# Kernel tuning notes

Hardware: AMD Instinct MI355X
Metric: run time of the kernel (lower is better)

The kernel has to match this reference:

```python
import jax, jax.numpy as jnp
import numpy as np

K = 3; PAD = 1; CIN = 64; COUT = 64; B = 4; H = 128; W = 128


def setup_inputs() -> dict:
    key = jax.random.key(0)
    k1, k2, k3 = jax.random.split(key, 3)
    x = jax.random.normal(k1, (B, CIN, H, W), dtype=jnp.float32)
    # offset-predicting conv: [2*K*K, Cin, K, K]; small init -> sub-pixel offsets
    w_off = jax.random.normal(k2, (2 * K * K, CIN, K, K), dtype=jnp.float32) * 0.01
    b_off = jnp.zeros((2 * K * K,), dtype=jnp.float32)
    # deformable conv weight (bias=False): [Cout, Cin, K, K]
    w_def = jax.random.normal(k3, (COUT, CIN, K, K), dtype=jnp.float32) * 0.05
    return {"x": x, "w_off": w_off, "b_off": b_off, "w_def": w_def}


def _deform_conv(x, w_off, b_off, w_def):
    Bb, Cin, Hh, Ww = x.shape
    KK = K * K
    # 1) predict offsets with a regular 3x3 conv (stride 1, pad 1)
    off = jax.lax.conv_general_dilated(
        x, w_off, window_strides=(1, 1), padding=[(PAD, PAD), (PAD, PAD)],
        dimension_numbers=("NCHW", "OIHW", "NCHW"))
    off = off + b_off[None, :, None, None]          # [B, 2*KK, H, W]
    off = off.reshape(Bb, KK, 2, Hh, Ww)            # torchvision layout: (dy, dx) per tap
    dy, dx = off[:, :, 0], off[:, :, 1]             # [B, KK, H, W]

    # 2) sampling coordinates: p = p0 + p_k + offset
    ky = (jnp.arange(KK) // K).astype(x.dtype)
    kx = (jnp.arange(KK) % K).astype(x.dtype)
    hh = jnp.arange(Hh, dtype=x.dtype)
    ww = jnp.arange(Ww, dtype=x.dtype)
    py = hh[None, None, :, None] - PAD + ky[None, :, None, None] + dy   # [B,KK,H,W]
    px = ww[None, None, None, :] - PAD + kx[None, :, None, None] + dx

    # 3) bilinear sampling with zero padding outside the image
    y0f = jnp.floor(py); x0f = jnp.floor(px)
    fy = py - y0f; fx = px - x0f
    y0 = y0f.astype(jnp.int32); x0 = x0f.astype(jnp.int32)
    x_flat = x.reshape(Bb, Cin, Hh * Ww)

    def gather(yi, xi):
        valid = (yi >= 0) & (yi < Hh) & (xi >= 0) & (xi < Ww)
        idx = jnp.clip(yi, 0, Hh - 1) * Ww + jnp.clip(xi, 0, Ww - 1)     # [B,KK,H,W]
        g = jax.vmap(lambda xf, ix: xf[:, ix.reshape(-1)])(x_flat, idx)  # [B,Cin,KK*H*W]
        return g.reshape(Bb, Cin, KK, Hh, Ww) * valid[:, None].astype(x.dtype)

    sampled = (gather(y0, x0)         * ((1 - fy) * (1 - fx))[:, None]
             + gather(y0, x0 + 1)     * ((1 - fy) * fx)[:, None]
             + gather(y0 + 1, x0)     * (fy * (1 - fx))[:, None]
             + gather(y0 + 1, x0 + 1) * (fy * fx)[:, None])               # [B,Cin,KK,H,W]

    # 4) convolution accumulation over (Cin, kernel taps)
    return jnp.einsum('bckhw,ock->bohw', sampled, w_def.reshape(COUT, Cin, KK))


def reference(x, w_off, b_off, w_def):
    return _deform_conv(x, w_off, b_off, w_def)
```

## Files before the change

kernel.cpp:

```cpp
#include <hip/hip_runtime.h>
#include <hip/hip_fp16.h>

#define Bn   4
#define CINc 64
#define COUTc 64
#define Hn   128
#define Wn   128
#define HW   (Hn * Wn)
#define KKc  9
#define NOFF 18

typedef short bf16x8 __attribute__((ext_vector_type(8)));
typedef float f32x4  __attribute__((ext_vector_type(4)));
typedef float f32x2  __attribute__((ext_vector_type(2)));

__device__ inline unsigned short f2bf(float f) {
    unsigned int u = __float_as_uint(f);
    return (unsigned short)((u + 0x7fffu + ((u >> 16) & 1u)) >> 16);
}

__device__ inline void dma16(const void* g, void* l) {
#if __has_builtin(__builtin_amdgcn_global_load_lds)
    __builtin_amdgcn_global_load_lds(
        (__attribute__((address_space(1))) void*)(g),
        (__attribute__((address_space(3))) void*)(l), 16, 0, 0);
#else
    *(uint4*)l = *(const uint4*)g;
#endif
}

__global__ __launch_bounds__(256) void prep_all(
        const float* __restrict__ x, unsigned short* __restrict__ xt,
        const float* __restrict__ w_off, const float* __restrict__ w_def,
        unsigned short* __restrict__ wkb_sw, unsigned short* __restrict__ wob_sw) {
    int gb = blockIdx.x;
    int t  = threadIdx.x;
    if (gb < 1024) {
        __shared__ float s[64][65];
        int half = gb & 1;
        int h    = (gb >> 1) & 127;
        int b    = gb >> 8;
        int w0   = half * 64;

        const float* xb = x + (size_t)b * CINc * HW + (size_t)h * Wn + w0;
        int c0 = t >> 4, wq = (t & 15) * 4;
        #pragma unroll
        for (int i = 0; i < 4; ++i) {
            int c = c0 + i * 16;
            float4 v = *(const float4*)(xb + (size_t)c * HW + wq);
            s[c][wq]     = v.x;
            s[c][wq + 1] = v.y;
            s[c][wq + 2] = v.z;
            s[c][wq + 3] = v.w;
        }
        __syncthreads();

        int cpair = t & 31, pxg = t >> 5;
        unsigned* xtp = (unsigned*)xt;
        #pragma unroll
        for (int i = 0; i < 8; ++i) {
            int px = pxg * 8 + i;
            float v0 = s[cpair * 2][px], v1 = s[cpair * 2 + 1][px];
            unsigned d = (unsigned)f2bf(v0) | ((unsigned)f2bf(v1) << 16);
            xtp[(((size_t)(b * Hn + h) * Wn) + w0 + px) * 32 + cpair] = d;
        }
        return;
    }
    int idx = (gb - 1024) * 256 + t;
    if (idx < 36864) {
        int j = idx & 7, l = (idx >> 3) & 63, s = idx >> 9;
        int k = s >> 3, kc = (s >> 2) & 1, ot = s & 3;
        int l15 = l & 15, quad = l >> 4;
        int o = ot * 16 + l15, c = kc * 32 + quad * 8 + j;
        wkb_sw[idx] = f2bf(w_def[((size_t)o * 64 + c) * 9 + k]);
    }
    int i2 = idx - 36864;
    if (i2 >= 0 && i2 < 18432) {
        int j = i2 & 7, l = (i2 >> 3) & 63, s = i2 >> 9;
        int tt = s >> 2, kc = (s >> 1) & 1, mt = s & 1;
        int l15 = l & 15, quad = l >> 4;
        int m = mt * 16 + l15, c = kc * 32 + quad * 8 + j;
        unsigned short v = 0;
        if (m < NOFF) v = f2bf(w_off[((size_t)m * 64 + c) * 9 + tt]);
        wob_sw[i2] = v;
    }
}


#define BFBUILD(C, kc, BF, W0, W1, W2, W3)                                   \
    do {                                                                     \
        const unsigned* t0 = (const unsigned*)&(C)[(kc) * 4 + 0];            \
        const unsigned* t1 = (const unsigned*)&(C)[(kc) * 4 + 1];            \
        const unsigned* b0 = (const unsigned*)&(C)[(kc) * 4 + 2];            \
        const unsigned* b1 = (const unsigned*)&(C)[(kc) * 4 + 3];            \
        _Pragma("unroll")                                                    \
        for (int jd = 0; jd < 4; ++jd) {                                     \
            f32x2 t0p = {__uint_as_float(t0[jd] << 16),                      \
                         __uint_as_float(t0[jd] & 0xFFFF0000u)};             \
            f32x2 t1p = {__uint_as_float(t1[jd] << 16),                      \
                         __uint_as_float(t1[jd] & 0xFFFF0000u)};             \
            f32x2 b0p = {__uint_as_float(b0[jd] << 16),                      \
                         __uint_as_float(b0[jd] & 0xFFFF0000u)};             \
            f32x2 b1p = {__uint_as_float(b1[jd] << 16),                      \
                         __uint_as_float(b1[jd] & 0xFFFF0000u)};             \
            f32x2 vv = t0p * (W0) + t1p * (W1) + b0p * (W2) + b1p * (W3);    \
            unsigned pk;                                                     \
            asm("v_cvt_pk_bf16_f32 %0, %1, %2"                               \
                : "=v"(pk) : "v"(vv.x), "v"(vv.y));                          \
            (BF).u[jd] = pk;                                                 \
        }                                                                    \
    } while (0)

#define TAP(k)                                                               \
    do {                                                                     \
        const uint4* C = R[(k) & 1];                                         \
        union { unsigned u; __half2 hv; } c01, c23;                          \
        c01.u = pw01[(k)]; c23.u = pw23[(k)];                                \
        float W0 = __low2float(c01.hv), W1 = __high2float(c01.hv);           \
        float W2 = __low2float(c23.hv), W3 = __high2float(c23.hv);           \
        union { bf16x8 v; unsigned u[4]; } bfa, bfb;                         \
        BFBUILD(C, 0, bfa, W0, W1, W2, W3);                                  \
        BFBUILD(C, 1, bfb, W0, W1, W2, W3);                                  \
        _Pragma("unroll")                                                    \
        for (int ot = 0; ot < 4; ++ot) {                                     \
            bf16x8 af0 = s_w[(((k) * 2 + 0) * 4 + ot + 36) * 64 + lane];     \
            acc[ot] = __builtin_amdgcn_mfma_f32_16x16x32_bf16(               \
                af0, bfa.v, acc[ot], 0, 0, 0);                               \
            bf16x8 af1 = s_w[(((k) * 2 + 1) * 4 + ot + 36) * 64 + lane];     \
            acc[ot] = __builtin_amdgcn_mfma_f32_16x16x32_bf16(               \
                af1, bfb.v, acc[ot], 0, 0, 0);                               \
        }                                                                    \
    } while (0)

#define FETCH(kk, st)                                                \
    do {                                                             \
        unsigned ad_ = ad[kk];                                       \
        unsigned xc_ = ad_ >> 16;                                    \
        unsigned at_ = (((ad_ & 255u) << 7) + xc_) << 6;             \
        unsigned ab_ = ((((ad_ >> 8) & 255u) << 7) + xc_) << 6;      \
        R[st][0] = *(const uint4*)(xtb + at_ + co0);                 \
        R[st][1] = *(const uint4*)(xtb + at_ + 64 + co0);            \
        R[st][2] = *(const uint4*)(xtb + ab_ + co0);                 \
        R[st][3] = *(const uint4*)(xtb + ab_ + 64 + co0);            \
        R[st][4] = *(const uint4*)(xtb + at_ + co1);                 \
        R[st][5] = *(const uint4*)(xtb + at_ + 64 + co1);            \
        R[st][6] = *(const uint4*)(xtb + ab_ + co1);                 \
        R[st][7] = *(const uint4*)(xtb + ab_ + 64 + co1);            \
    } while (0)

__global__ __launch_bounds__(512, 2) void fused_deform_v19(
        const unsigned short* __restrict__ xt,
        const unsigned short* __restrict__ wob_sw,
        const unsigned short* __restrict__ wkb_sw,
        const float* __restrict__ b_off, float* __restrict__ out) {
    extern __shared__ bf16x8 s_w[];

    int gid  = blockIdx.x;
    int tid  = threadIdx.x;
    int lane = tid & 63;
    int wave = __builtin_amdgcn_readfirstlane(tid >> 6);
    int l15  = lane & 15;
    int quad = lane >> 4;

    #pragma unroll
    for (int i = 0; i < 14; ++i) {
        int seg = i * 8 + wave;
        if (seg < 108) {
            const uint4* src = (seg < 36)
                ? (const uint4*)wob_sw + (size_t)seg * 64 + lane
                : (const uint4*)wkb_sw + (size_t)(seg - 36) * 64 + lane;
            dma16(src, (char*)s_w + (size_t)seg * 1024);
        }
    }

    bool first = true;
    #pragma unroll 1
    for (int row = 0; row < 2; ++row) {
        int gv   = gid + row * 256;
        int xcd  = gv & 7;
        int j    = gv >> 3;
        int hh   = j & 15;
        int b    = j >> 4;
        int h    = xcd * 16 + hh;
        int p    = wave * 16 + l15;

        uint4 L[9][2];
        unsigned msk[9];
        const unsigned short* xtb = xt + (size_t)b * HW * 64;
        #pragma unroll
        for (int t9 = 0; t9 < 9; ++t9) {
            int ty = t9 / 3, tx = t9 % 3;
            int y  = h - 1 + ty;
            int xg = p - 1 + tx;
            bool v = (y >= 0) && (y < Hn) && (xg >= 0) && (xg < Wn);
            msk[t9] = v ? 0xFFFFFFFFu : 0u;
            int yc = min(max(y, 0), Hn - 1);
            int xc = min(max(xg, 0), Wn - 1);
            size_t base = ((size_t)yc * Wn + xc) * 64;
            L[t9][0] = *(const uint4*)(xtb + base + quad * 8);
            L[t9][1] = *(const uint4*)(xtb + base + 32 + quad * 8);
        }
        if (first) {
            __syncthreads();
            first = false;
        }

        f32x4 oa0 = (f32x4){0.f, 0.f, 0.f, 0.f};
        f32x4 oa1 = (f32x4){0.f, 0.f, 0.f, 0.f};
        #pragma unroll
        for (int t9 = 0; t9 < 9; ++t9) {
            unsigned m = msk[t9];
            #pragma unroll
            for (int kc = 0; kc < 2; ++kc) {
                union { bf16x8 v; uint4 u; } bf;
                bf.u = L[t9][kc];
                bf.u.x &= m; bf.u.y &= m; bf.u.z &= m; bf.u.w &= m;
                bf16x8 a0 = s_w[((t9 * 2 + kc) * 2 + 0) * 64 + lane];
                bf16x8 a1 = s_w[((t9 * 2 + kc) * 2 + 1) * 64 + lane];
                oa0 = __builtin_amdgcn_mfma_f32_16x16x32_bf16(a0, bf.v, oa0, 0, 0, 0);
                oa1 = __builtin_amdgcn_mfma_f32_16x16x32_bf16(a1, bf.v, oa1, 0, 0, 0);
            }
        }

        unsigned my_ad[3]  = {0, 0, 0};
        unsigned my_w01[3] = {0, 0, 0};
        unsigned my_w23[3] = {0, 0, 0};
        auto phase1 = [&](int k, float dy, float dx, int slot) {
            float py  = (float)(h - 1 + k / 3) + dy;
            float pxf = (float)(p - 1 + k % 3) + dx;
            float y0f = floorf(py), x0f = floorf(pxf);
            float fy = py - y0f, fx = pxf - x0f;
            int y0 = (int)y0f, x0 = (int)x0f;
            bool vy0 = (y0 >= 0) & (y0 < Hn);
            bool vy1 = (y0 + 1 >= 0) & (y0 + 1 < Hn);
            bool vx0 = (x0 >= 0) & (x0 < Wn);
            bool vx1 = (x0 + 1 >= 0) & (x0 + 1 < Wn);
            float wy0 = vy0 ? 1.f - fy : 0.f;
            float wy1 = vy1 ? fy : 0.f;
            float wx0 = vx0 ? 1.f - fx : 0.f;
            float wx1 = vx1 ? fx : 0.f;
            int xc = min(max(x0, 0), Wn - 2);
            bool sel0 = (min(max(x0, 0), Wn - 1) != xc);
            bool sel1 = ((min(max(x0 + 1, 0), Wn - 1) - xc) == 1);
            float Wa = (sel0 ? 0.f : wx0) + (sel1 ? 0.f : wx1);
            float Wb = (sel0 ? wx0 : 0.f) + (sel1 ? wx1 : 0.f);
            int yc0 = min(max(y0, 0), Hn - 1), yc1 = min(max(y0 + 1, 0), Hn - 1);
            union { __half2 hv; unsigned u; } c01, c23;
            c01.hv = __floats2half2_rn(wy0 * Wa, wy0 * Wb);
            c23.hv = __floats2half2_rn(wy1 * Wa, wy1 * Wb);
            my_ad[slot]  = (unsigned)yc0 | ((unsigned)yc1 << 8) | ((unsigned)xc << 16);
            my_w01[slot] = c01.u;
            my_w23[slot] = c23.u;
        };
        int kb = quad * 2;
        phase1(kb,     oa0[0] + b_off[4 * quad],     oa0[1] + b_off[4 * quad + 1], 0);
        phase1(kb + 1, oa0[2] + b_off[4 * quad + 2], oa0[3] + b_off[4 * quad + 3], 1);
        if (quad == 0)
            phase1(8, oa1[0] + b_off[16], oa1[1] + b_off[17], 2);

        unsigned ad[KKc], pw01[KKc], pw23[KKc];
        #pragma unroll
        for (int k = 0; k < KKc; ++k) {
            int src  = (k < 8) ? ((k >> 1) * 16 + l15) : l15;
            int slot = (k < 8) ? (k & 1) : 2;
            ad[k]   = (unsigned)__shfl((int)my_ad[slot],  src, 64);
            pw01[k] = (unsigned)__shfl((int)my_w01[slot], src, 64);
            pw23[k] = (unsigned)__shfl((int)my_w23[slot], src, 64);
        }

        f32x4 acc[4];
        #pragma unroll
        for (int ot = 0; ot < 4; ++ot) acc[ot] = (f32x4){0.f, 0.f, 0.f, 0.f};

        uint4 R[2][8];
        int co0 = quad * 8, co1 = 32 + quad * 8;

        FETCH(0, 0);
        FETCH(1, 1); TAP(0);
        FETCH(2, 0); TAP(1);
        FETCH(3, 1); TAP(2);
        FETCH(4, 0); TAP(3);
        FETCH(5, 1); TAP(4);
        FETCH(6, 0); TAP(5);
        FETCH(7, 1); TAP(6);
        FETCH(8, 0); TAP(7);
        TAP(8);

        #pragma unroll
        for (int ot = 0; ot < 4; ++ot)
            #pragma unroll
            for (int rr = 0; rr < 4; ++rr) {
                int o = ot * 16 + quad * 4 + rr;
                out[(((size_t)b * COUTc + o) * Hn + h) * Wn + p] = acc[ot][rr];
            }
    }
}

extern "C" void kernel_launch(void* const* d_in, const int* in_sizes, int n_in,
                              void* d_out, int out_size, void* d_ws, size_t ws_size,
                              hipStream_t stream) {
    const float* x     = (const float*)d_in[0];
    const float* w_off = (const float*)d_in[1];
    const float* b_off = (const float*)d_in[2];
    const float* w_def = (const float*)d_in[3];
    float* out = (float*)d_out;

    char* ws = (char*)d_ws;
    unsigned short* xt = (unsigned short*)ws;
    ws += (size_t)Bn * HW * CINc * sizeof(unsigned short);
    unsigned short* wkb_sw = (unsigned short*)ws;
    ws += 36864 * sizeof(unsigned short);
    unsigned short* wob_sw = (unsigned short*)ws;

    static bool attr_set = false;
    if (!attr_set) {
        (void)hipFuncSetAttribute((const void*)fused_deform_v19,
                                  hipFuncAttributeMaxDynamicSharedMemorySize,
                                  110592);
        attr_set = true;
    }

    prep_all<<<1024 + 216, 256, 0, stream>>>(x, xt, w_off, w_def, wkb_sw, wob_sw);
    fused_deform_v19<<<256, 512, 110592, stream>>>(xt, wob_sw, wkb_sw, b_off, out);
}
```

Baseline: 116.5 us.

## Stage 5-row input halo in LDS and gather bilinear samples from shared memory

Each block now processes one output row and first copies a swizzled 5-row x 128-column x 64-channel bf16 halo of the input into LDS via async DMA. Both the offset conv and the deformable sampling read from LDS. A wave-level check falls back to global gathers when any sampled row lies outside the halo. The offset-conv weights and deform weights now share one LDS region that is reloaded between phases. LDS use grows to 152 KB, which likely means one block per CU, and the block count doubles with no row loop inside each block.

```diff
diff --git a/kernel.cpp b/kernel.cpp
--- a/kernel.cpp
+++ b/kernel.cpp
@@ -123,16 +123,16 @@
         BFBUILD(C, 1, bfb, W0, W1, W2, W3);                                  \
         _Pragma("unroll")                                                    \
         for (int ot = 0; ot < 4; ++ot) {                                     \
-            bf16x8 af0 = s_w[(((k) * 2 + 0) * 4 + ot + 36) * 64 + lane];     \
+            bf16x8 af0 = s_wv[(((k) * 2 + 0) * 4 + ot) * 64 + lane];         \
             acc[ot] = __builtin_amdgcn_mfma_f32_16x16x32_bf16(               \
                 af0, bfa.v, acc[ot], 0, 0, 0);                               \
-            bf16x8 af1 = s_w[(((k) * 2 + 1) * 4 + ot + 36) * 64 + lane];     \
+            bf16x8 af1 = s_wv[(((k) * 2 + 1) * 4 + ot) * 64 + lane];         \
             acc[ot] = __builtin_amdgcn_mfma_f32_16x16x32_bf16(               \
                 af1, bfb.v, acc[ot], 0, 0, 0);                               \
         }                                                                    \
     } while (0)
 
-#define FETCH(kk, st)                                                \
+#define FETCH_G(kk, st)                                              \
     do {                                                             \
         unsigned ad_ = ad[kk];                                       \
         unsigned xc_ = ad_ >> 16;                                    \
@@ -148,152 +148,202 @@
         R[st][7] = *(const uint4*)(xtb + ab_ + 64 + co1);            \
     } while (0)
 
-__global__ __launch_bounds__(512, 2) void fused_deform_v19(
+#define FETCH_L(kk, st)                                              \
+    do {                                                             \
+        unsigned ad_ = ad[kk];                                       \
+        int xc_ = (int)(ad_ >> 16);                                  \
+        int r0_ = (int)(ad_ & 255u) - h + 2;                         \
+        int r1_ = (int)((ad_ >> 8) & 255u) - h + 2;                  \
+        int b00 = (r0_ * 128 + xc_) * 128;                           \
+        int b10 = (r1_ * 128 + xc_) * 128;                           \
+        int j0  = (quad ^ (xc_ & 7)) << 4;                           \
+        int j1  = (quad ^ ((xc_ + 1) & 7)) << 4;                     \
+        int j0b = ((4 + quad) ^ (xc_ & 7)) << 4;                     \
+        int j1b = ((4 + quad) ^ ((xc_ + 1) & 7)) << 4;               \
+        R[st][0] = *(const uint4*)(s_mem + b00 + j0);                \
+        R[st][1] = *(const uint4*)(s_mem + b00 + 128 + j1);          \
+        R[st][2] = *(const uint4*)(s_mem + b10 + j0);                \
+        R[st][3] = *(const uint4*)(s_mem + b10 + 128 + j1);          \
+        R[st][4] = *(const uint4*)(s_mem + b00 + j0b);               \
+        R[st][5] = *(const uint4*)(s_mem + b00 + 128 + j1b);         \
+        R[st][6] = *(const uint4*)(s_mem + b10 + j0b);               \
+        R[st][7] = *(const uint4*)(s_mem + b10 + 128 + j1b);         \
+    } while (0)
+
+__global__ __launch_bounds__(512, 2) void fused_deform_v20(
         const unsigned short* __restrict__ xt,
         const unsigned short* __restrict__ wob_sw,
         const unsigned short* __restrict__ wkb_sw,
         const float* __restrict__ b_off, float* __restrict__ out) {
-    extern __shared__ bf16x8 s_w[];
+    extern __shared__ char s_mem[];
+    bf16x8* s_wv = (bf16x8*)(s_mem + 81920);
 
     int gid  = blockIdx.x;
+    int xcd  = gid & 7;
+    int j    = gid >> 3;
+    int hh   = j & 15;
+    int b    = j >> 4;
+    int h    = xcd * 16 + hh;
     int tid  = threadIdx.x;
     int lane = tid & 63;
     int wave = __builtin_amdgcn_readfirstlane(tid >> 6);
     int l15  = lane & 15;
     int quad = lane >> 4;
-
-    #pragma unroll
-    for (int i = 0; i < 14; ++i) {
+    int p    = wave * 16 + l15;
+
+    const unsigned short* xtb = xt + (size_t)b * HW * 64;
+
+    int xl = lane >> 3;
+    int sl = lane & 7;
+    #pragma unroll
+    for (int i = 0; i < 10; ++i) {
+        int slot = i * 8 + wave;
+        int r  = slot >> 4;
+        int g  = slot & 15;
+        int y  = min(max(h - 2 + r, 0), Hn - 1);
+        int xx = g * 8 + xl;
+        int jj = sl ^ (xx & 7);
+        dma16(xtb + ((size_t)y * Wn + xx) * 64 + jj * 8,
+              s_mem + (size_t)r * 16384 + (size_t)g * 1024);
+    }
+    #pragma unroll
+    for (int i = 0; i < 5; ++i) {
         int seg = i * 8 + wave;
-        if (seg < 108) {
-            const uint4* src = (seg < 36)
-                ? (const uint4*)wob_sw + (size_t)seg * 64 + lane
-                : (const uint4*)wkb_sw + (size_t)(seg - 36) * 64 + lane;
-            dma16(src, (char*)s_w + (size_t)seg * 1024);
+        if (seg < 36)
+            dma16((const uint4*)wob_sw + seg * 64 + lane,
+                  s_mem + 81920 + (size_t)seg * 1024);
+    }
+    __syncthreads();
+
+    f32x4 oa0 = (f32x4){0.f, 0.f, 0.f, 0.f};
+    f32x4 oa1 = (f32x4){0.f, 0.f, 0.f, 0.f};
+    #pragma unroll
+    for (int t9 = 0; t9 < 9; ++t9) {
+        int ty = t9 / 3, tx = t9 % 3;
+        int y  = h - 1 + ty;
+        int xg = p - 1 + tx;
+        bool v = (y >= 0) && (y < Hn) && (xg >= 0) && (xg < Wn);
+        unsigned m = v ? 0xFFFFFFFFu : 0u;
+        int yc = min(max(y, 0), Hn - 1);
+        int xc = min(max(xg, 0), Wn - 1);
+        int r  = yc - h + 2;
+        int base = (r * 128 + xc) * 128;
+        uint4 L0 = *(const uint4*)(s_mem + base + ((quad ^ (xc & 7)) << 4));
+        uint4 L1 = *(const uint4*)(s_mem + base + (((4 + quad) ^ (xc & 7)) << 4));
+        #pragma unroll
+        for (int kc = 0; kc < 2; ++kc) {
+            union { bf16x8 v; uint4 u; } bf;
+            bf.u = kc ? L1 : L0;
+            bf.u.x &= m; bf.u.y &= m; bf.u.z &= m; bf.u.w &= m;
+            bf16x8 a0 = s_wv[((t9 * 2 + kc) * 2 + 0) * 64 + lane];
+            bf16x8 a1 = s_wv[((t9 * 2 + kc) * 2 + 1) * 64 + lane];
+            oa0 = __builtin_amdgcn_mfma_f32_16x16x32_bf16(a0, bf.v, oa0, 0, 0, 0);
+            oa1 = __builtin_amdgcn_mfma_f32_16x16x32_bf16(a1, bf.v, oa1, 0, 0, 0);
         }
     }
 
-    bool first = true;
-    #pragma unroll 1
-    for (int row = 0; row < 2; ++row) {
-        int gv   = gid + row * 256;
-        int xcd  = gv & 7;
-        int j    = gv >> 3;
-        int hh   = j & 15;
-        int b    = j >> 4;
-        int h    = xcd * 16 + hh;
-        int p    = wave * 16 + l15;
-
-        uint4 L[9][2];
-        unsigned msk[9];
-        const unsigned short* xtb = xt + (size_t)b * HW * 64;
+    unsigned my_ad[3]  = {0, 0, 0};
+    unsigned my_w01[3] = {0, 0, 0};
+    unsigned my_w23[3] = {0, 0, 0};
+    auto phase1 = [&](int k, float dy, float dx, int slot) {
+        float py  = (float)(h - 1 + k / 3) + dy;
+        float pxf = (float)(p - 1 + k % 3) + dx;
+        float y0f = floorf(py), x0f = floorf(pxf);
+        float fy = py - y0f, fx = pxf - x0f;
+        int y0 = (int)y0f, x0 = (int)x0f;
+        bool vy0 = (y0 >= 0) & (y0 < Hn);
+        bool vy1 = (y0 + 1 >= 0) & (y0 + 1 < Hn);
+        bool vx0 = (x0 >= 0) & (x0 < Wn);
+        bool vx1 = (x0 + 1 >= 0) & (x0 + 1 < Wn);
+        float wy0 = vy0 ? 1.f - fy : 0.f;
+        float wy1 = vy1 ? fy : 0.f;
+        float wx0 = vx0 ? 1.f - fx : 0.f;
+        float wx1 = vx1 ? fx : 0.f;
+        int xc = min(max(x0, 0), Wn - 2);
+        bool sel0 = (min(max(x0, 0), Wn - 1) != xc);
+        bool sel1 = ((min(max(x0 + 1, 0), Wn - 1) - xc) == 1);
+        float Wa = (sel0 ? 0.f : wx0) + (sel1 ? 0.f : wx1);
+        float Wb = (sel0 ? wx0 : 0.f) + (sel1 ? wx1 : 0.f);
+        int yc0 = min(max(y0, 0), Hn - 1), yc1 = min(max(y0 + 1, 0), Hn - 1);
+        union { __half2 hv; unsigned u; } c01, c23;
+        c01.hv = __floats2half2_rn(wy0 * Wa, wy0 * Wb);
+        c23.hv = __floats2half2_rn(wy1 * Wa, wy1 * Wb);
+        my_ad[slot]  = (unsigned)yc0 | ((unsigned)yc1 << 8) | ((unsigned)xc << 16);
+        my_w01[slot] = c01.u;
+        my_w23[slot] = c23.u;
+    };
+    int kb = quad * 2;
+    phase1(kb,     oa0[0] + b_off[4 * quad],     oa0[1] + b_off[4 * quad + 1], 0);
+    phase1(kb + 1, oa0[2] + b_off[4 * quad + 2], oa0[3] + b_off[4 * quad + 3], 1);
+    if (quad == 0)
+        phase1(8, oa1[0] + b_off[16], oa1[1] + b_off[17], 2);
+    __syncthreads();
+
+    #pragma unroll
+    for (int i = 0; i < 9; ++i) {
+        int seg = i * 8 + wave;
+        dma16((const uint4*)wkb_sw + (size_t)seg * 64 + lane,
+              s_mem + 81920 + (size_t)seg * 1024);
+    }
+
+    unsigned ad[KKc], pw01[KKc], pw23[KKc];
+    #pragma unroll
+    for (int k = 0; k < KKc; ++k) {
+        int src  = (k < 8) ? ((k >> 1) * 16 + l15) : l15;
+        int slot = (k < 8) ? (k & 1) : 2;
+        ad[k]   = (unsigned)__shfl((int)my_ad[slot],  src, 64);
+        pw01[k] = (unsigned)__shfl((int)my_w01[slot], src, 64);
+        pw23[k] = (unsigned)__shfl((int)my_w23[slot], src, 64);
+    }
+    __syncthreads();
+
+    bool oow = false;
+    #pragma unroll
+    for (int k = 0; k < KKc; ++k) {
+        int r0 = (int)(ad[k] & 255u) - h + 2;
+        int r1 = (int)((ad[k] >> 8) & 255u) - h + 2;
+        oow |= ((unsigned)r0 > 4u) | ((unsigned)r1 > 4u);
+    }
+    bool use_global = __any(oow);
+
+    f32x4 acc[4];
+    #pragma unroll
+    for (int ot = 0; ot < 4; ++ot) acc[ot] = (f32x4){0.f, 0.f, 0.f, 0.f};
+
+    uint4 R[2][8];
+    int co0 = quad * 8, co1 = 32 + quad * 8;
+
+    if (__builtin_expect(use_global, 0)) {
+        FETCH_G(0, 0);
+        FETCH_G(1, 1); TAP(0);
+        FETCH_G(2, 0); TAP(1);
+        FETCH_G(3, 1); TAP(2);
+        FETCH_G(4, 0); TAP(3);
+        FETCH_G(5, 1); TAP(4);
+        FETCH_G(6, 0); TAP(5);
+        FETCH_G(7, 1); TAP(6);
+        FETCH_G(8, 0); TAP(7);
+        TAP(8);
+    } else {
+        FETCH_L(0, 0);
+        FETCH_L(1, 1); TAP(0);
+        FETCH_L(2, 0); TAP(1);
+        FETCH_L(3, 1); TAP(2);
+        FETCH_L(4, 0); TAP(3);
+        FETCH_L(5, 1); TAP(4);
+        FETCH_L(6, 0); TAP(5);
+        FETCH_L(7, 1); TAP(6);
+        FETCH_L(8, 0); TAP(7);
+        TAP(8);
+    }
+
+    #pragma unroll
+    for (int ot = 0; ot < 4; ++ot)
         #pragma unroll
-        for (int t9 = 0; t9 < 9; ++t9) {
-            int ty = t9 / 3, tx = t9 % 3;
-            int y  = h - 1 + ty;
-            int xg = p - 1 + tx;
-            bool v = (y >= 0) && (y < Hn) && (xg >= 0) && (xg < Wn);
-            msk[t9] = v ? 0xFFFFFFFFu : 0u;
-            int yc = min(max(y, 0), Hn - 1);
-            int xc = min(max(xg, 0), Wn - 1);
-            size_t base = ((size_t)yc * Wn + xc) * 64;
-            L[t9][0] = *(const uint4*)(xtb + base + quad * 8);
-            L[t9][1] = *(const uint4*)(xtb + base + 32 + quad * 8);
+        for (int rr = 0; rr < 4; ++rr) {
+            int o = ot * 16 + quad * 4 + rr;
+            out[(((size_t)b * COUTc + o) * Hn + h) * Wn + p] = acc[ot][rr];
         }
-        if (first) {
-            __syncthreads();
-            first = false;
-        }
-
-        f32x4 oa0 = (f32x4){0.f, 0.f, 0.f, 0.f};
-        f32x4 oa1 = (f32x4){0.f, 0.f, 0.f, 0.f};
-        #pragma unroll
-        for (int t9 = 0; t9 < 9; ++t9) {
-            unsigned m = msk[t9];
-            #pragma unroll
-            for (int kc = 0; kc < 2; ++kc) {
-                union { bf16x8 v; uint4 u; } bf;
-                bf.u = L[t9][kc];
-                bf.u.x &= m; bf.u.y &= m; bf.u.z &= m; bf.u.w &= m;
-                bf16x8 a0 = s_w[((t9 * 2 + kc) * 2 + 0) * 64 + lane];
-                bf16x8 a1 = s_w[((t9 * 2 + kc) * 2 + 1) * 64 + lane];
-                oa0 = __builtin_amdgcn_mfma_f32_16x16x32_bf16(a0, bf.v, oa0, 0, 0, 0);
-                oa1 = __builtin_amdgcn_mfma_f32_16x16x32_bf16(a1, bf.v, oa1, 0, 0, 0);
-            }
-        }
-
-        unsigned my_ad[3]  = {0, 0, 0};
-        unsigned my_w01[3] = {0, 0, 0};
-        unsigned my_w23[3] = {0, 0, 0};
-        auto phase1 = [&](int k, float dy, float dx, int slot) {
-            float py  = (float)(h - 1 + k / 3) + dy;
-            float pxf = (float)(p - 1 + k % 3) + dx;
-            float y0f = floorf(py), x0f = floorf(pxf);
-            float fy = py - y0f, fx = pxf - x0f;
-            int y0 = (int)y0f, x0 = (int)x0f;
-            bool vy0 = (y0 >= 0) & (y0 < Hn);
-            bool vy1 = (y0 + 1 >= 0) & (y0 + 1 < Hn);
-            bool vx0 = (x0 >= 0) & (x0 < Wn);
-            bool vx1 = (x0 + 1 >= 0) & (x0 + 1 < Wn);
-            float wy0 = vy0 ? 1.f - fy : 0.f;
-            float wy1 = vy1 ? fy : 0.f;
-            float wx0 = vx0 ? 1.f - fx : 0.f;
-            float wx1 = vx1 ? fx : 0.f;
-            int xc = min(max(x0, 0), Wn - 2);
-            bool sel0 = (min(max(x0, 0), Wn - 1) != xc);
-            bool sel1 = ((min(max(x0 + 1, 0), Wn - 1) - xc) == 1);
-            float Wa = (sel0 ? 0.f : wx0) + (sel1 ? 0.f : wx1);
-            float Wb = (sel0 ? wx0 : 0.f) + (sel1 ? wx1 : 0.f);
-            int yc0 = min(max(y0, 0), Hn - 1), yc1 = min(max(y0 + 1, 0), Hn - 1);
-            union { __half2 hv; unsigned u; } c01, c23;
-            c01.hv = __floats2half2_rn(wy0 * Wa, wy0 * Wb);
-            c23.hv = __floats2half2_rn(wy1 * Wa, wy1 * Wb);
-            my_ad[slot]  = (unsigned)yc0 | ((unsigned)yc1 << 8) | ((unsigned)xc << 16);
-            my_w01[slot] = c01.u;
-            my_w23[slot] = c23.u;
-        };
-        int kb = quad * 2;
-        phase1(kb,     oa0[0] + b_off[4 * quad],     oa0[1] + b_off[4 * quad + 1], 0);
-        phase1(kb + 1, oa0[2] + b_off[4 * quad + 2], oa0[3] + b_off[4 * quad + 3], 1);
-        if (quad == 0)
-            phase1(8, oa1[0] + b_off[16], oa1[1] + b_off[17], 2);
-
-        unsigned ad[KKc], pw01[KKc], pw23[KKc];
-        #pragma unroll
-        for (int k = 0; k < KKc; ++k) {
-            int src  = (k < 8) ? ((k >> 1) * 16 + l15) : l15;
-            int slot = (k < 8) ? (k & 1) : 2;
-            ad[k]   = (unsigned)__shfl((int)my_ad[slot],  src, 64);
-            pw01[k] = (unsigned)__shfl((int)my_w01[slot], src, 64);
-            pw23[k] = (unsigned)__shfl((int)my_w23[slot], src, 64);
-        }
-
-        f32x4 acc[4];
-        #pragma unroll
-        for (int ot = 0; ot < 4; ++ot) acc[ot] = (f32x4){0.f, 0.f, 0.f, 0.f};
-
-        uint4 R[2][8];
-        int co0 = quad * 8, co1 = 32 + quad * 8;
-
-        FETCH(0, 0);
-        FETCH(1, 1); TAP(0);
-        FETCH(2, 0); TAP(1);
-        FETCH(3, 1); TAP(2);
-        FETCH(4, 0); TAP(3);
-        FETCH(5, 1); TAP(4);
-        FETCH(6, 0); TAP(5);
-        FETCH(7, 1); TAP(6);
-        FETCH(8, 0); TAP(7);
-        TAP(8);
-
-        #pragma unroll
-        for (int ot = 0; ot < 4; ++ot)
-            #pragma unroll
-            for (int rr = 0; rr < 4; ++rr) {
-                int o = ot * 16 + quad * 4 + rr;
-                out[(((size_t)b * COUTc + o) * Hn + h) * Wn + p] = acc[ot][rr];
-            }
-    }
 }
 
 extern "C" void kernel_launch(void* const* d_in, const int* in_sizes, int n_in,
@@ -314,12 +364,12 @@
 
     static bool attr_set = false;
     if (!attr_set) {
-        (void)hipFuncSetAttribute((const void*)fused_deform_v19,
+        (void)hipFuncSetAttribute((const void*)fused_deform_v20,
                                   hipFuncAttributeMaxDynamicSharedMemorySize,
-                                  110592);
+                                  155648);
         attr_set = true;
     }
 
     prep_all<<<1024 + 216, 256, 0, stream>>>(x, xt, w_off, w_def, wkb_sw, wob_sw);
-    fused_deform_v19<<<256, 512, 110592, stream>>>(xt, wob_sw, wkb_sw, b_off, out);
-}
+    fused_deform_v20<<<Bn * Hn, 512, 155648, stream>>>(xt, wob_sw, wkb_sw, b_off, out);
+}
```

Result: faster. 97.12 us (-16.6%).
